# Optimization experiments

Hardware: AMD Instinct MI355X
Metric: run time of the kernel (lower is better)

## Reference

```python
import jax, jax.numpy as jnp
import numpy as np


def setup_inputs() -> dict:
    key = jax.random.key(0)
    ks = jax.random.split(key, 7)
    B, S, D_IN, D_K, D_V = 4, 4096, 1024, 64, 64
    s = 1.0 / np.sqrt(D_IN)
    return {
        "query": jax.random.normal(ks[0], (B, S, D_IN), jnp.float32),
        "key": jax.random.normal(ks[1], (B, S, D_IN), jnp.float32),
        "value": jax.random.normal(ks[2], (B, S, D_IN), jnp.float32),
        "Wq": jax.random.normal(ks[3], (D_IN, D_K), jnp.float32) * s,
        "bq": jnp.zeros((D_K,), jnp.float32),
        "Wk": jax.random.normal(ks[4], (D_IN, D_K), jnp.float32) * s,
        "bk": jnp.zeros((D_K,), jnp.float32),
        "Wv": jax.random.normal(ks[5], (D_IN, D_V), jnp.float32) * s,
        "bv": jnp.zeros((D_V,), jnp.float32),
    }


def reference(query, key, value, Wq, bq, Wk, bk, Wv, bv):
    # q(query) is computed twice in the original but is identical; compute once.
    q = query @ Wq + bq            # [B,S,dk]
    k = key @ Wk + bk              # [B,S,dk]
    v = value @ Wv + bv            # [B,S,dv]
    scale = jnp.asarray(q.shape[-1] ** 0.5, q.dtype)
    scores = jnp.einsum("bqd,bkd->bqk", q, k) / scale  # [B,S,S]
    probs = jax.nn.softmax(scores, axis=-1)
    return jnp.einsum("bqk,bkd->bqd", probs, v)        # [B,S,dv]
```

## Files before the change

### kernel.cpp

```cpp
#include <hip/hip_runtime.h>
#include <cmath>

constexpr int B_  = 4;
constexpr int S_  = 4096;
constexpr int DIN = 1024;
constexpr int DH  = 64;

typedef short bf16x8 __attribute__((ext_vector_type(8)));
typedef float f32x4  __attribute__((ext_vector_type(4)));

#define GPTR(p) (const __attribute__((address_space(1))) unsigned int*)(p)
#define LPTR(p) (__attribute__((address_space(3))) unsigned int*)(p)

__device__ __forceinline__ ushort f2bf(float x) {
    unsigned int u = __float_as_uint(x);
    return (ushort)((u + 0x7FFFu + ((u >> 16) & 1u)) >> 16);
}

__device__ __forceinline__ bf16x8 cvt8(float4 a, float4 b) {
    union { bf16x8 v; ushort u[8]; } r;
    r.u[0] = f2bf(a.x); r.u[1] = f2bf(a.y); r.u[2] = f2bf(a.z); r.u[3] = f2bf(a.w);
    r.u[4] = f2bf(b.x); r.u[5] = f2bf(b.y); r.u[6] = f2bf(b.z); r.u[7] = f2bf(b.w);
    return r.v;
}

#define QSCALE 0.18033688011112042f

__global__ __launch_bounds__(256) void setup_w(
    const float* __restrict__ Wq, const float* __restrict__ Wk,
    const float* __restrict__ Wv, ushort* __restrict__ Wt_g)
{
    const int y = blockIdx.y;
    const float* W = (y == 0) ? Wq : (y == 1) ? Wk : Wv;
    const int g   = blockIdx.x * 256 + threadIdx.x;
    const int p   = g & 7;
    const int n   = (g >> 3) & 63;
    const int win = g >> 9;
    const int c   = p ^ (n & 7);
    const int k0  = win * 64 + c * 8;
    union { uint4 q; ushort u[8]; } r;
    #pragma unroll
    for (int i = 0; i < 8; ++i) r.u[i] = f2bf(W[(size_t)(k0 + i) * DH + n]);
    *(uint4*)(Wt_g + ((size_t)y << 16) + (size_t)(((win * 64 + n) * 8 + p) * 8)) = r.q;
}

__global__ __launch_bounds__(256) void proj_kernel(
    const float* __restrict__ Xq, const float* __restrict__ Xk, const float* __restrict__ Xv,
    const float* __restrict__ bq, const float* __restrict__ bk, const float* __restrict__ bv,
    const ushort* __restrict__ Wt_g,
    ushort* __restrict__ Qb, ushort* __restrict__ Kb, ushort* __restrict__ Vt)
{
    const int y = blockIdx.y;
    const float *X, *bias;
    if (y == 0)      { X = Xq; bias = bq; }
    else if (y == 1) { X = Xk; bias = bk; }
    else             { X = Xv; bias = bv; }

    __shared__ ushort Wlds[2][4096];

    const int tid  = threadIdx.x;
    const int w    = tid >> 6;
    const int lane = tid & 63;
    const int m    = lane & 15;
    const int quad = lane >> 4;
    const int row0 = blockIdx.x * 64;

    const size_t  xrow = (size_t)(row0 + w * 16 + m) * DIN;
    const ushort* wsrc = Wt_g + ((size_t)y << 16);

    float bias_v[4];
    #pragma unroll
    for (int nt = 0; nt < 4; ++nt) bias_v[nt] = bias[nt * 16 + m];

    f32x4 acc[4] = {};

    #pragma unroll
    for (int i = 0; i < 2; ++i) {
        const int chunk = w * 2 + i;
        __builtin_amdgcn_global_load_lds(GPTR(wsrc + chunk * 512 + lane * 8),
                                         LPTR(&Wlds[0][chunk * 512]), 16, 0, 0);
    }
    float4 cur[4], nxt[4];
    {
        const float* px = X + xrow + quad * 8;
        cur[0] = *(const float4*)(px);      cur[1] = *(const float4*)(px + 4);
        cur[2] = *(const float4*)(px + 32); cur[3] = *(const float4*)(px + 36);
    }
    __syncthreads();

    for (int it = 0; it < 16; ++it) {
        if (it < 15) {
            #pragma unroll
            for (int i = 0; i < 2; ++i) {
                const int chunk = w * 2 + i;
                __builtin_amdgcn_global_load_lds(
                    GPTR(wsrc + (it + 1) * 4096 + chunk * 512 + lane * 8),
                    LPTR(&Wlds[(it + 1) & 1][chunk * 512]), 16, 0, 0);
            }
            const float* px = X + xrow + (it + 1) * 64 + quad * 8;
            nxt[0] = *(const float4*)(px);      nxt[1] = *(const float4*)(px + 4);
            nxt[2] = *(const float4*)(px + 32); nxt[3] = *(const float4*)(px + 36);
        }
        const ushort* buf = Wlds[it & 1];
        #pragma unroll
        for (int ks = 0; ks < 2; ++ks) {
            const bf16x8 a = cvt8(cur[ks * 2], cur[ks * 2 + 1]);
            #pragma unroll
            for (int nt = 0; nt < 4; ++nt) {
                const int n = nt * 16 + m;
                const int p = (ks * 4 + quad) ^ (m & 7);
                const bf16x8 bfr = *(const bf16x8*)&buf[n * 64 + p * 8];
                acc[nt] = __builtin_amdgcn_mfma_f32_16x16x32_bf16(a, bfr, acc[nt], 0, 0, 0);
            }
        }
        __syncthreads();
        #pragma unroll
        for (int i = 0; i < 4; ++i) cur[i] = nxt[i];
    }

    if (y < 2) {
        ushort* Out = (y == 0) ? Qb : Kb;
        const float sc = (y == 0) ? QSCALE : 1.0f;
        #pragma unroll
        for (int nt = 0; nt < 4; ++nt)
            #pragma unroll
            for (int j = 0; j < 4; ++j) {
                const int row = row0 + w * 16 + quad * 4 + j;
                Out[(size_t)row * DH + nt * 16 + m] = f2bf((acc[nt][j] + bias_v[nt]) * sc);
            }
    } else {
        ushort* Vx = (ushort*)Wlds;
        #pragma unroll
        for (int nt = 0; nt < 4; ++nt)
            #pragma unroll
            for (int j = 0; j < 4; ++j) {
                const int d = nt * 16 + m;
                const int s = w * 16 + quad * 4 + j;
                Vx[d * 72 + (((s >> 3) ^ (d & 7)) * 8) + (s & 7)] = f2bf(acc[nt][j] + bias_v[nt]);
            }
        __syncthreads();
        const int batch = row0 >> 12;
        const int s0    = row0 & 4095;
        for (int i = tid; i < 512; i += 256) {
            const int d = i >> 3, c = i & 7;
            const uint4 v = *(const uint4*)&Vx[d * 72 + ((c ^ (d & 7)) * 8)];
            *(uint4*)(Vt + ((size_t)batch * 64 + d) * S_ + s0 + c * 8) = v;
        }
    }
}

__global__ __launch_bounds__(256, 4) void attn_kernel(
    const ushort* __restrict__ Qb, const ushort* __restrict__ Kb,
    const ushort* __restrict__ Vt, float* __restrict__ Opart, float* __restrict__ Lpart)
{
    __shared__ ushort Ks[64 * 64];
    __shared__ ushort Vs[64 * 64];
    __shared__ ushort Pt[64 * 72];

    const int tid  = threadIdx.x;
    const int w    = tid >> 6;
    const int lane = tid & 63;
    const int m    = lane & 15;
    const int quad = lane >> 4;
    const int b    = blockIdx.z, jc = blockIdx.y, qt = blockIdx.x;
    const int q0   = qt * 64;

    bf16x8 qf[2];
    #pragma unroll
    for (int ks = 0; ks < 2; ++ks)
        qf[ks] = *(const bf16x8*)(Qb + (size_t)(b * S_ + q0 + w * 16 + m) * 64
                                     + ks * 32 + quad * 8);

    f32x4 acc_o[4] = {};
    float Lp[4] = {};

    const ushort* kbase = Kb + (size_t)b * S_ * 64;
    const ushort* vbase = Vt + (size_t)b * 64 * S_;

    for (int it = 0; it < 16; ++it) {
        const int jt = jc * 16 + it;
        __syncthreads();
        #pragma unroll
        for (int i = 0; i < 2; ++i) {
            const int slot = w * 128 + i * 64 + lane;
            const int j = slot >> 3, c = slot & 7;
            __builtin_amdgcn_global_load_lds(
                GPTR(kbase + (size_t)(jt * 64 + j) * 64 + ((c ^ (j & 7)) * 8)),
                LPTR(&Ks[(w * 128 + i * 64) * 8]), 16, 0, 0);
            __builtin_amdgcn_global_load_lds(
                GPTR(vbase + (size_t)j * S_ + jt * 64 + ((c ^ (j & 7)) * 8)),
                LPTR(&Vs[(w * 128 + i * 64) * 8]), 16, 0, 0);
        }
        __syncthreads();

        f32x4 acc_s[4] = {};
        #pragma unroll
        for (int ks = 0; ks < 2; ++ks)
            #pragma unroll
            for (int jt4 = 0; jt4 < 4; ++jt4) {
                const int j = jt4 * 16 + m;
                const bf16x8 kf = *(const bf16x8*)&Ks[j * 64 + (((ks * 4 + quad) ^ (j & 7)) * 8)];
                acc_s[jt4] = __builtin_amdgcn_mfma_f32_16x16x32_bf16(
                    qf[ks], kf, acc_s[jt4], 0, 0, 0);
            }

        #pragma unroll
        for (int jt4 = 0; jt4 < 4; ++jt4)
            #pragma unroll
            for (int r = 0; r < 4; ++r) {
                const float e = exp2f(acc_s[jt4][r]);
                Lp[r] += e;
                Pt[(w * 16 + quad * 4 + r) * 72 + jt4 * 16 + m] = f2bf(e);
            }

        #pragma unroll
        for (int jc2 = 0; jc2 < 2; ++jc2) {
            const bf16x8 pf = *(const bf16x8*)&Pt[(w * 16 + m) * 72 + jc2 * 32 + quad * 8];
            #pragma unroll
            for (int dt = 0; dt < 4; ++dt) {
                const int d = dt * 16 + m;
                const bf16x8 vf = *(const bf16x8*)&Vs[d * 64 + (((jc2 * 4 + quad) ^ (d & 7)) * 8)];
                acc_o[dt] = __builtin_amdgcn_mfma_f32_16x16x32_bf16(pf, vf, acc_o[dt], 0, 0, 0);
            }
        }
    }

    #pragma unroll
    for (int r = 0; r < 4; ++r) {
        float s = Lp[r];
        #pragma unroll
        for (int off = 1; off < 16; off <<= 1)
            s += __shfl_xor(s, off, 64);
        Lp[r] = s;
    }

    const size_t bj = (size_t)(b * 4 + jc);
    float* Ob = Opart + (bj << 18);
    #pragma unroll
    for (int dt = 0; dt < 4; ++dt)
        #pragma unroll
        for (int r = 0; r < 4; ++r) {
            const int row = q0 + w * 16 + quad * 4 + r;
            Ob[(size_t)row * 64 + dt * 16 + m] = acc_o[dt][r];
        }
    if (m == 0) {
        #pragma unroll
        for (int r = 0; r < 4; ++r)
            Lpart[bj * 4096 + q0 + w * 16 + quad * 4 + r] = Lp[r];
    }
}

__global__ __launch_bounds__(256) void reduce_kernel(
    const float* __restrict__ Opart, const float* __restrict__ Lpart, float* __restrict__ out)
{
    const int g    = blockIdx.x * 256 + threadIdx.x;
    const int base = g << 2;
    const int b    = base >> 18;
    const int rem  = base & 0x3FFFF;
    const int q    = rem >> 6;
    float4 o = make_float4(0.f, 0.f, 0.f, 0.f);
    float  l = 0.f;
    #pragma unroll
    for (int jcc = 0; jcc < 4; ++jcc) {
        const float4 p = *(const float4*)(Opart + (((size_t)(b * 4 + jcc)) << 18) + rem);
        o.x += p.x; o.y += p.y; o.z += p.z; o.w += p.w;
        l += Lpart[(size_t)(b * 4 + jcc) * 4096 + q];
    }
    const float inv = 1.0f / l;
    o.x *= inv; o.y *= inv; o.z *= inv; o.w *= inv;
    *(float4*)(out + base) = o;
}

extern "C" void kernel_launch(void* const* d_in, const int* in_sizes, int n_in,
                              void* d_out, int out_size, void* d_ws, size_t ws_size,
                              hipStream_t stream)
{
    const float* query = (const float*)d_in[0];
    const float* key_  = (const float*)d_in[1];
    const float* value = (const float*)d_in[2];
    const float* Wq    = (const float*)d_in[3];
    const float* bq    = (const float*)d_in[4];
    const float* Wk    = (const float*)d_in[5];
    const float* bk    = (const float*)d_in[6];
    const float* Wv    = (const float*)d_in[7];
    const float* bv    = (const float*)d_in[8];
    float* out = (float*)d_out;

    char* ws = (char*)d_ws;
    ushort* Qb    = (ushort*)(ws);
    ushort* Kb    = (ushort*)(ws + (2  << 20));
    ushort* Vt    = (ushort*)(ws + (4  << 20));
    float*  Opart = (float*) (ws + (6  << 20));
    float*  Lpart = (float*) (ws + (22 << 20));
    ushort* Wt_g  = (ushort*)(ws + (6  << 20));

    setup_w<<<dim3(32, 3), 256, 0, stream>>>(Wq, Wk, Wv, Wt_g);
    proj_kernel<<<dim3(256, 3), 256, 0, stream>>>(
        query, key_, value, bq, bk, bv, Wt_g, Qb, Kb, Vt);
    attn_kernel<<<dim3(64, 4, 4), 256, 0, stream>>>(Qb, Kb, Vt, Opart, Lpart);
    reduce_kernel<<<dim3(1024), 256, 0, stream>>>(Opart, Lpart, out);
}
```

Measured before the change: 265.0 us.

## Double-buffer K/V tiles in attention and feed projection weights from global

The attention kernel now double-buffers the K and V tiles in LDS. It issues the async global-to-LDS copy for the next tile before computing on the current one, which cuts one barrier per iteration and overlaps load latency with the MFMA work. The projection kernel drops LDS staging of the weight tile and loads the weight fragments straight from global memory, which is L2-resident, into registers. That requires removing the XOR swizzle in the weight pre-layout kernel. Launch bounds move to 3 waves per SIMD to fit the larger LDS footprint, so occupancy may drop.

```diff
diff --git a/kernel.cpp b/kernel.cpp
--- a/kernel.cpp
+++ b/kernel.cpp
@@ -36,15 +36,14 @@
     const int p   = g & 7;
     const int n   = (g >> 3) & 63;
     const int win = g >> 9;
-    const int c   = p ^ (n & 7);
-    const int k0  = win * 64 + c * 8;
+    const int k0  = win * 64 + p * 8;
     union { uint4 q; ushort u[8]; } r;
     #pragma unroll
     for (int i = 0; i < 8; ++i) r.u[i] = f2bf(W[(size_t)(k0 + i) * DH + n]);
     *(uint4*)(Wt_g + ((size_t)y << 16) + (size_t)(((win * 64 + n) * 8 + p) * 8)) = r.q;
 }
 
-__global__ __launch_bounds__(256) void proj_kernel(
+__global__ __launch_bounds__(256, 3) void proj_kernel(
     const float* __restrict__ Xq, const float* __restrict__ Xk, const float* __restrict__ Xv,
     const float* __restrict__ bq, const float* __restrict__ bk, const float* __restrict__ bv,
     const ushort* __restrict__ Wt_g,
@@ -56,7 +55,7 @@
     else if (y == 1) { X = Xk; bias = bk; }
     else             { X = Xv; bias = bv; }
 
-    __shared__ ushort Wlds[2][4096];
+    __shared__ ushort Vx[64 * 72];
 
     const int tid  = threadIdx.x;
     const int w    = tid >> 6;
@@ -65,8 +64,8 @@
     const int quad = lane >> 4;
     const int row0 = blockIdx.x * 64;
 
-    const size_t  xrow = (size_t)(row0 + w * 16 + m) * DIN;
-    const ushort* wsrc = Wt_g + ((size_t)y << 16);
+    const size_t  xrow  = (size_t)(row0 + w * 16 + m) * DIN;
+    const ushort* wbase = Wt_g + ((size_t)y << 16);
 
     float bias_v[4];
     #pragma unroll
@@ -74,46 +73,33 @@
 
     f32x4 acc[4] = {};
 
-    #pragma unroll
-    for (int i = 0; i < 2; ++i) {
-        const int chunk = w * 2 + i;
-        __builtin_amdgcn_global_load_lds(GPTR(wsrc + chunk * 512 + lane * 8),
-                                         LPTR(&Wlds[0][chunk * 512]), 16, 0, 0);
-    }
     float4 cur[4], nxt[4];
     {
         const float* px = X + xrow + quad * 8;
         cur[0] = *(const float4*)(px);      cur[1] = *(const float4*)(px + 4);
         cur[2] = *(const float4*)(px + 32); cur[3] = *(const float4*)(px + 36);
     }
-    __syncthreads();
 
     for (int it = 0; it < 16; ++it) {
+        bf16x8 wf[2][4];
+        #pragma unroll
+        for (int ks = 0; ks < 2; ++ks)
+            #pragma unroll
+            for (int nt = 0; nt < 4; ++nt)
+                wf[ks][nt] = *(const bf16x8*)(wbase
+                    + (size_t)(((it * 64 + nt * 16 + m) * 8 + ks * 4 + quad) * 8));
         if (it < 15) {
-            #pragma unroll
-            for (int i = 0; i < 2; ++i) {
-                const int chunk = w * 2 + i;
-                __builtin_amdgcn_global_load_lds(
-                    GPTR(wsrc + (it + 1) * 4096 + chunk * 512 + lane * 8),
-                    LPTR(&Wlds[(it + 1) & 1][chunk * 512]), 16, 0, 0);
-            }
             const float* px = X + xrow + (it + 1) * 64 + quad * 8;
             nxt[0] = *(const float4*)(px);      nxt[1] = *(const float4*)(px + 4);
             nxt[2] = *(const float4*)(px + 32); nxt[3] = *(const float4*)(px + 36);
         }
-        const ushort* buf = Wlds[it & 1];
         #pragma unroll
         for (int ks = 0; ks < 2; ++ks) {
             const bf16x8 a = cvt8(cur[ks * 2], cur[ks * 2 + 1]);
             #pragma unroll
-            for (int nt = 0; nt < 4; ++nt) {
-                const int n = nt * 16 + m;
-                const int p = (ks * 4 + quad) ^ (m & 7);
-                const bf16x8 bfr = *(const bf16x8*)&buf[n * 64 + p * 8];
-                acc[nt] = __builtin_amdgcn_mfma_f32_16x16x32_bf16(a, bfr, acc[nt], 0, 0, 0);
-            }
-        }
-        __syncthreads();
+            for (int nt = 0; nt < 4; ++nt)
+                acc[nt] = __builtin_amdgcn_mfma_f32_16x16x32_bf16(a, wf[ks][nt], acc[nt], 0, 0, 0);
+        }
         #pragma unroll
         for (int i = 0; i < 4; ++i) cur[i] = nxt[i];
     }
@@ -129,7 +115,6 @@
                 Out[(size_t)row * DH + nt * 16 + m] = f2bf((acc[nt][j] + bias_v[nt]) * sc);
             }
     } else {
-        ushort* Vx = (ushort*)Wlds;
         #pragma unroll
         for (int nt = 0; nt < 4; ++nt)
             #pragma unroll
@@ -149,12 +134,12 @@
     }
 }
 
-__global__ __launch_bounds__(256, 4) void attn_kernel(
+__global__ __launch_bounds__(256, 3) void attn_kernel(
     const ushort* __restrict__ Qb, const ushort* __restrict__ Kb,
     const ushort* __restrict__ Vt, float* __restrict__ Opart, float* __restrict__ Lpart)
 {
-    __shared__ ushort Ks[64 * 64];
-    __shared__ ushort Vs[64 * 64];
+    __shared__ ushort Ks[2][4096];
+    __shared__ ushort Vs[2][4096];
     __shared__ ushort Pt[64 * 72];
 
     const int tid  = threadIdx.x;
@@ -177,21 +162,33 @@
     const ushort* kbase = Kb + (size_t)b * S_ * 64;
     const ushort* vbase = Vt + (size_t)b * 64 * S_;
 
+    const int slot0 = w * 128 + lane;
+    const int j0 = slot0 >> 3, c0 = slot0 & 7;
+    const int j1 = (slot0 + 64) >> 3, c1 = (slot0 + 64) & 7;
+
+    #define ISSUE_DMA(IT, NB)                                                          \
+        do {                                                                           \
+            const int _jt = jc * 16 + (IT);                                            \
+            __builtin_amdgcn_global_load_lds(                                          \
+                GPTR(kbase + (size_t)(_jt * 64 + j0) * 64 + ((c0 ^ (j0 & 7)) * 8)),    \
+                LPTR(&Ks[NB][(w * 128) * 8]), 16, 0, 0);                               \
+            __builtin_amdgcn_global_load_lds(                                          \
+                GPTR(kbase + (size_t)(_jt * 64 + j1) * 64 + ((c1 ^ (j1 & 7)) * 8)),    \
+                LPTR(&Ks[NB][(w * 128 + 64) * 8]), 16, 0, 0);                          \
+            __builtin_amdgcn_global_load_lds(                                          \
+                GPTR(vbase + (size_t)j0 * S_ + _jt * 64 + ((c0 ^ (j0 & 7)) * 8)),      \
+                LPTR(&Vs[NB][(w * 128) * 8]), 16, 0, 0);                               \
+            __builtin_amdgcn_global_load_lds(                                          \
+                GPTR(vbase + (size_t)j1 * S_ + _jt * 64 + ((c1 ^ (j1 & 7)) * 8)),      \
+                LPTR(&Vs[NB][(w * 128 + 64) * 8]), 16, 0, 0);                          \
+        } while (0)
+
+    ISSUE_DMA(0, 0);
+
     for (int it = 0; it < 16; ++it) {
-        const int jt = jc * 16 + it;
         __syncthreads();
-        #pragma unroll
-        for (int i = 0; i < 2; ++i) {
-            const int slot = w * 128 + i * 64 + lane;
-            const int j = slot >> 3, c = slot & 7;
-            __builtin_amdgcn_global_load_lds(
-                GPTR(kbase + (size_t)(jt * 64 + j) * 64 + ((c ^ (j & 7)) * 8)),
-                LPTR(&Ks[(w * 128 + i * 64) * 8]), 16, 0, 0);
-            __builtin_amdgcn_global_load_lds(
-                GPTR(vbase + (size_t)j * S_ + jt * 64 + ((c ^ (j & 7)) * 8)),
-                LPTR(&Vs[(w * 128 + i * 64) * 8]), 16, 0, 0);
-        }
-        __syncthreads();
+        if (it < 15) ISSUE_DMA(it + 1, (it + 1) & 1);
+        const int cb = it & 1;
 
         f32x4 acc_s[4] = {};
         #pragma unroll
@@ -199,7 +196,7 @@
             #pragma unroll
             for (int jt4 = 0; jt4 < 4; ++jt4) {
                 const int j = jt4 * 16 + m;
-                const bf16x8 kf = *(const bf16x8*)&Ks[j * 64 + (((ks * 4 + quad) ^ (j & 7)) * 8)];
+                const bf16x8 kf = *(const bf16x8*)&Ks[cb][j * 64 + (((ks * 4 + quad) ^ (j & 7)) * 8)];
                 acc_s[jt4] = __builtin_amdgcn_mfma_f32_16x16x32_bf16(
                     qf[ks], kf, acc_s[jt4], 0, 0, 0);
             }
@@ -219,11 +216,12 @@
             #pragma unroll
             for (int dt = 0; dt < 4; ++dt) {
                 const int d = dt * 16 + m;
-                const bf16x8 vf = *(const bf16x8*)&Vs[d * 64 + (((jc2 * 4 + quad) ^ (d & 7)) * 8)];
+                const bf16x8 vf = *(const bf16x8*)&Vs[cb][d * 64 + (((jc2 * 4 + quad) ^ (d & 7)) * 8)];
                 acc_o[dt] = __builtin_amdgcn_mfma_f32_16x16x32_bf16(pf, vf, acc_o[dt], 0, 0, 0);
             }
         }
     }
+    #undef ISSUE_DMA
 
     #pragma unroll
     for (int r = 0; r < 4; ++r) {
```

Measured after the change: 286.6 us. 1.08x slower.
